# Kernel optimization log

Hardware: AMD Instinct MI355X
Metric: run time of the kernel (lower is better)

Reference implementation:

```python
import jax, jax.numpy as jnp
import numpy as np

N = 256
ACTION_DIM = 32
BATCH = 64
SEQ = 128
J0 = -0.1
J1 = 0.1
ALPHA = 0.15  # hard-coded in forward()


def _initial_bump(batch, num_neurons, bump_width_factor=10):
    # create_initial_bump with initial_angle = pi for every batch element
    angles = jnp.full((batch,), jnp.pi, dtype=jnp.float32)
    centers = (angles * num_neurons / (2.0 * jnp.pi))[:, None]          # [B,1]
    width = num_neurons / bump_width_factor
    idx = jnp.arange(num_neurons, dtype=jnp.float32)[None, :]          # [1,N]
    d = jnp.abs(idx - centers)
    dist = jnp.minimum(d, num_neurons - d)                             # circular distance
    bump = jnp.exp(-(dist ** 2) / (2.0 * width ** 2))
    return bump / jnp.linalg.norm(bump, axis=1, keepdims=True)          # [B,N]


def _w_delta7(num_neurons):
    idx = jnp.arange(num_neurons, dtype=jnp.float32)
    angle_diff = 2.0 * jnp.pi * (idx[:, None] - idx[None, :]) / num_neurons
    return jnp.cos(angle_diff)                                          # [N,N]


def setup_inputs() -> dict:
    key = jax.random.key(0)
    k1, k2, k3 = jax.random.split(key, 3)
    action_signal = jax.random.normal(k1, (BATCH, SEQ, ACTION_DIM), dtype=jnp.float32)
    scale = 1.0 / np.sqrt(N).astype(np.float32)
    Wo = jax.random.normal(k2, (N, N), dtype=jnp.float32) * scale
    Wa = jax.random.normal(k3, (ACTION_DIM, N, N), dtype=jnp.float32) * scale
    return {"action_signal": action_signal, "Wo": Wo, "Wa": Wa}


def reference(action_signal, Wo, Wa):
    B, T, A = action_signal.shape
    n = Wo.shape[0]
    r0 = _initial_bump(B, n)          # [B,N]
    Wd7 = _w_delta7(n)                # [N,N]

    def step(r, a_t):
        # W_eff = J0 + J1*Wo + sum_a a_t[:,a] * Wa[a]; recurrent = r @ W_eff
        # r @ (J0 * ones) == J0 * sum(r) broadcast -> avoid materializing [B,N,N]
        rec = (J0 * jnp.sum(r, axis=-1, keepdims=True)
               + J1 * (r @ Wo)
               + jnp.einsum('bn,anm,ba->bm', r, Wa, a_t))
        r_new = (1.0 - ALPHA) * r + ALPHA * jax.nn.relu(rec)
        return r_new, r_new

    _, bump = jax.lax.scan(step, r0, jnp.swapaxes(action_signal, 0, 1))  # [T,B,N]
    bump = jnp.swapaxes(bump, 0, 1)                                      # [B,T,N]
    r_delta7 = bump @ Wd7                                                # [B,T,N]
    r_history = r_delta7 / jnp.max(r_delta7, axis=2, keepdims=True)
    return r_history, bump
```

## Files before the change

### kernel.cpp

```cpp
#include <hip/hip_runtime.h>
#include <math.h>

#define NN 256
#define AD 32
#define BB 64
#define TT 128
#define KJ0 (-0.1f)
#define KJ1 (0.1f)
#define KALPHA 0.15f
#define BUMP_OFF (BB*TT*NN)

#define RSTR 284
#define LDS_WM   0
#define LDS_WW   32768
#define LDS_RL   33792
#define LDS_CF   38336
#define LDS_RED  38848
#define LDS_SUMR 39872
#define LDS_FLOATS 39888

#define BAR_STRIDE 64

__global__ void __launch_bounds__(256) ring_init(unsigned* bar) {
  bar[threadIdx.x] = 0u;
}

__device__ __forceinline__ void group_barrier(unsigned* g, unsigned phase) {
  __syncthreads();
  if (threadIdx.x == 0) {
    unsigned old = __hip_atomic_fetch_add(&g[0], 1u, __ATOMIC_ACQ_REL, __HIP_MEMORY_SCOPE_AGENT);
    if (old == 63u) {
      __hip_atomic_store(&g[0], 0u, __ATOMIC_RELAXED, __HIP_MEMORY_SCOPE_AGENT);
      __hip_atomic_store(&g[32], phase, __ATOMIC_RELEASE, __HIP_MEMORY_SCOPE_AGENT);
    } else {
      const unsigned long long t0 = __builtin_amdgcn_s_memrealtime();
      while (__hip_atomic_load(&g[32], __ATOMIC_RELAXED, __HIP_MEMORY_SCOPE_AGENT) < phase) {
        __builtin_amdgcn_s_sleep(2);
        if (__builtin_amdgcn_s_memrealtime() - t0 > 1000000ull) break;
      }
      (void)__hip_atomic_load(&g[32], __ATOMIC_ACQUIRE, __HIP_MEMORY_SCOPE_AGENT);
    }
  }
  __syncthreads();
}

__global__ void __launch_bounds__(1024) ring_main(const float* __restrict__ act,
                                                  const float* __restrict__ Wo,
                                                  const float* __restrict__ Wa,
                                                  float* __restrict__ out,
                                                  unsigned* __restrict__ bar) {
  extern __shared__ float sm[];
  const int tid = threadIdx.x;
  const int bid = blockIdx.x;
  const int bt = bid >> 6;
  const int mt = bid & 63;
  const int wv = tid >> 6;
  const int ln = tid & 63;
  const int bg = ln & 3;
  const int ks = wv*16 + (ln >> 2);
  const int a_idx = ks >> 3;
  const int sub = ks & 7;
  unsigned* barg = bar + bt*BAR_STRIDE;

  #pragma unroll
  for (int j = 0; j < 8; ++j) {
    const int flat = j*1024 + tid;
    const int i = flat >> 8, kk = flat & 255;
    const int a = kk >> 3, n = ((kk & 7) << 5) + i;
    const float4 w = *(const float4*)(Wa + (a*NN + n)*NN + (mt<<2));
    *(float4*)(&sm[LDS_WM + (flat<<2)]) = w;
  }
  if (tid < 256) {
    const float4 w = *(const float4*)(Wo + tid*NN + (mt<<2));
    float4 s; s.x = w.x*KJ1; s.y = w.y*KJ1; s.z = w.z*KJ1; s.w = w.w*KJ1;
    *(float4*)(&sm[LDS_WW + (tid<<2)]) = s;
  }

  {
    const int c = ln;
    float v0[4]; float ss = 0.f, sv = 0.f;
    const float denom = 2.0f*25.6f*25.6f;
    #pragma unroll
    for (int u = 0; u < 4; ++u) {
      const float fn = (float)(c*4 + u);
      const float d = fabsf(fn - 128.0f);
      const float dist = fminf(d, 256.0f - d);
      const float e = expf(-(dist*dist)/denom);
      v0[u] = e; ss += e*e; sv += e;
    }
    ss += __shfl_xor(ss,32); ss += __shfl_xor(ss,16); ss += __shfl_xor(ss,8);
    ss += __shfl_xor(ss,4);  ss += __shfl_xor(ss,2);  ss += __shfl_xor(ss,1);
    sv += __shfl_xor(sv,32); sv += __shfl_xor(sv,16); sv += __shfl_xor(sv,8);
    sv += __shfl_xor(sv,4);  sv += __shfl_xor(sv,2);  sv += __shfl_xor(sv,1);
    const float inv = 1.0f/sqrtf(ss);
    float4 o; o.x = v0[0]*inv; o.y = v0[1]*inv; o.z = v0[2]*inv; o.w = v0[3]*inv;
    *(float4*)(&sm[LDS_RL + wv*RSTR + (c<<2) + ((c>>3)<<2)]) = o;
    if (c == 0) sm[LDS_SUMR + wv] = sv*inv;
  }

  for (int t = 0; t < TT; ++t) {
    if (t > 0) {
      const float* src = out + BUMP_OFF + (((bt*16 + wv)*TT) + (t-1))*NN + (ln<<2);
      const float4 x = *(const float4*)src;
      *(float4*)(&sm[LDS_RL + wv*RSTR + (ln<<2) + ((ln>>3)<<2)]) = x;
      float s = x.x + x.y + x.z + x.w;
      s += __shfl_xor(s,32); s += __shfl_xor(s,16); s += __shfl_xor(s,8);
      s += __shfl_xor(s,4);  s += __shfl_xor(s,2);  s += __shfl_xor(s,1);
      if (ln == 0) sm[LDS_SUMR + wv] = s;
    }
    if (tid < 512) {
      const int b0 = tid >> 5, aa = tid & 31;
      sm[LDS_CF + aa*16 + b0] = act[(bt*16 + b0)*(TT*AD) + t*AD + aa];
    }
    __syncthreads();

    float acc[4][4];
    #pragma unroll
    for (int v = 0; v < 4; ++v) { acc[v][0]=0.f; acc[v][1]=0.f; acc[v][2]=0.f; acc[v][3]=0.f; }

    {
      const float4 w = *(const float4*)&sm[LDS_WW + (ks<<2)];
      const int np = ks + ((ks>>5)<<2);
      #pragma unroll
      for (int v = 0; v < 4; ++v) {
        const float rv = sm[LDS_RL + ((bg<<2)+v)*RSTR + np];
        acc[v][0] += rv*w.x; acc[v][1] += rv*w.y; acc[v][2] += rv*w.z; acc[v][3] += rv*w.w;
      }
    }

    float pacc[4][4];
    #pragma unroll
    for (int v = 0; v < 4; ++v) { pacc[v][0]=0.f; pacc[v][1]=0.f; pacc[v][2]=0.f; pacc[v][3]=0.f; }
    const float* wp  = &sm[LDS_WM + (ks<<2)];
    const float* rp0 = &sm[LDS_RL + (bg<<2)*RSTR + sub*36];
    const float* rp1 = rp0 + RSTR;
    const float* rp2 = rp1 + RSTR;
    const float* rp3 = rp2 + RSTR;
    #pragma unroll 2
    for (int i = 0; i < 32; i += 4) {
      const float4 w0 = *(const float4*)(wp + (i  )*1024);
      const float4 w1 = *(const float4*)(wp + (i+1)*1024);
      const float4 w2 = *(const float4*)(wp + (i+2)*1024);
      const float4 w3 = *(const float4*)(wp + (i+3)*1024);
      const float4 ra = *(const float4*)(rp0 + i);
      const float4 rb = *(const float4*)(rp1 + i);
      const float4 rc = *(const float4*)(rp2 + i);
      const float4 rd = *(const float4*)(rp3 + i);
      #pragma unroll
      for (int u = 0; u < 4; ++u) {
        const float4 w = (u==0)?w0:((u==1)?w1:((u==2)?w2:w3));
        const float r0v = (u==0)?ra.x:((u==1)?ra.y:((u==2)?ra.z:ra.w));
        const float r1v = (u==0)?rb.x:((u==1)?rb.y:((u==2)?rb.z:rb.w));
        const float r2v = (u==0)?rc.x:((u==1)?rc.y:((u==2)?rc.z:rc.w));
        const float r3v = (u==0)?rd.x:((u==1)?rd.y:((u==2)?rd.z:rd.w));
        pacc[0][0] += r0v*w.x; pacc[0][1] += r0v*w.y; pacc[0][2] += r0v*w.z; pacc[0][3] += r0v*w.w;
        pacc[1][0] += r1v*w.x; pacc[1][1] += r1v*w.y; pacc[1][2] += r1v*w.z; pacc[1][3] += r1v*w.w;
        pacc[2][0] += r2v*w.x; pacc[2][1] += r2v*w.y; pacc[2][2] += r2v*w.z; pacc[2][3] += r2v*w.w;
        pacc[3][0] += r3v*w.x; pacc[3][1] += r3v*w.y; pacc[3][2] += r3v*w.z; pacc[3][3] += r3v*w.w;
      }
    }
    #pragma unroll
    for (int v = 0; v < 4; ++v) {
      const float cva = sm[LDS_CF + a_idx*16 + (bg<<2) + v];
      acc[v][0] += cva*pacc[v][0]; acc[v][1] += cva*pacc[v][1];
      acc[v][2] += cva*pacc[v][2]; acc[v][3] += cva*pacc[v][3];
    }

    float vals[16];
    #pragma unroll
    for (int v = 0; v < 4; ++v) { vals[v*4+0]=acc[v][0]; vals[v*4+1]=acc[v][1];
                                  vals[v*4+2]=acc[v][2]; vals[v*4+3]=acc[v][3]; }
    { const bool hi = (ln & 32) != 0;
      #pragma unroll
      for (int j = 0; j < 8; ++j) { const float kp = hi?vals[j+8]:vals[j], sd = hi?vals[j]:vals[j+8];
        vals[j] = kp + __shfl_xor(sd, 32); } }
    { const bool hi = (ln & 16) != 0;
      #pragma unroll
      for (int j = 0; j < 4; ++j) { const float kp = hi?vals[j+4]:vals[j], sd = hi?vals[j]:vals[j+4];
        vals[j] = kp + __shfl_xor(sd, 16); } }
    { const bool hi = (ln & 8) != 0;
      #pragma unroll
      for (int j = 0; j < 2; ++j) { const float kp = hi?vals[j+2]:vals[j], sd = hi?vals[j]:vals[j+2];
        vals[j] = kp + __shfl_xor(sd, 8); } }
    { const bool hi = (ln & 4) != 0;
      { const float kp = hi?vals[1]:vals[0], sd = hi?vals[0]:vals[1];
        vals[0] = kp + __shfl_xor(sd, 4); } }
    sm[LDS_RED + wv*64 + ln] = vals[0];
    __syncthreads();

    if (wv == 0) {
      float tot = 0.f;
      #pragma unroll
      for (int w2 = 0; w2 < 16; ++w2) tot += sm[LDS_RED + w2*64 + ln];
      const int j = (((ln>>5)&1)<<3)|(((ln>>4)&1)<<2)|(((ln>>3)&1)<<1)|((ln>>2)&1);
      const int v = j >> 2, m = j & 3;
      const int b = (ln & 3)*4 + v;
      const int mm = (mt<<2) + m;
      const float rec  = tot + KJ0 * sm[LDS_SUMR + b];
      const float rold = sm[LDS_RL + b*RSTR + mm + ((mm>>5)<<2)];
      const float rnew = (1.0f-KALPHA)*rold + KALPHA*fmaxf(rec, 0.0f);
      out[BUMP_OFF + ((bt*16 + b)*TT + t)*NN + mm] = rnew;
    }
    if (t < TT-1) group_barrier(barg, (unsigned)(t+1));
  }
}

__global__ void __launch_bounds__(256) ring_epi(float* out) {
  const int b = blockIdx.x >> 7, t = blockIdx.x & 127;
  const int n = threadIdx.x;
  const int wv = threadIdx.x >> 6, ln = threadIdx.x & 63;
  __shared__ float l[12];
  const float v = out[BUMP_OFF + (b*TT + t)*NN + n];
  const float ang = (float)n * (6.283185307179586f/256.0f);
  const float cn = cosf(ang), sn = sinf(ang);
  float pc = v*cn, ps = v*sn;
  #pragma unroll
  for (int m = 32; m >= 1; m >>= 1) { pc += __shfl_xor(pc, m); ps += __shfl_xor(ps, m); }
  if (ln == 0) { l[wv] = pc; l[4+wv] = ps; }
  __syncthreads();
  const float C = l[0]+l[1]+l[2]+l[3];
  const float S = l[4]+l[5]+l[6]+l[7];
  const float d7 = C*cn + S*sn;
  float mx = d7;
  #pragma unroll
  for (int m = 32; m >= 1; m >>= 1) mx = fmaxf(mx, __shfl_xor(mx, m));
  if (ln == 0) l[8+wv] = mx;
  __syncthreads();
  mx = fmaxf(fmaxf(l[8], l[9]), fmaxf(l[10], l[11]));
  out[(b*TT + t)*NN + n] = d7/mx;
}

extern "C" void kernel_launch(void* const* d_in, const int* in_sizes, int n_in,
                              void* d_out, int out_size, void* d_ws, size_t ws_size,
                              hipStream_t stream) {
  const float* act = (const float*)d_in[0];
  const float* Wo  = (const float*)d_in[1];
  const float* Wa  = (const float*)d_in[2];
  float* outp = (float*)d_out;
  unsigned* bar = (unsigned*)d_ws;

  hipLaunchKernelGGL(ring_init, dim3(1), dim3(256), 0, stream, bar);

  (void)hipFuncSetAttribute(reinterpret_cast<const void*>(ring_main),
                            hipFuncAttributeMaxDynamicSharedMemorySize, LDS_FLOATS*4);

  hipLaunchKernelGGL(ring_main, dim3(256), dim3(1024), LDS_FLOATS*4, stream,
                     act, Wo, Wa, outp, bar);

  hipLaunchKernelGGL(ring_epi, dim3(BB*TT), dim3(256), 0, stream, outp);
}
```

Measured before the change: 1.699 ms.

## Replace counter barrier with per-block step flags polled by one wavefront

Replaces the centralized atomic-counter group barrier with per-block monotonically increasing step flags, padded to separate cache lines. Each block publishes its step with a release store. At the start of the next step, the 64 lanes of wave 0 each poll one peer block's flag. This removes the serialized atomic fetch-add contention and the last-arriver broadcast from the critical path of every timestep. The cost is 64 polling loads per block per step.

Measured after the change: 1.519 ms. -10.6%, faster.

```diff
diff --git a/kernel.cpp b/kernel.cpp
--- a/kernel.cpp
+++ b/kernel.cpp
@@ -19,36 +19,19 @@
 #define LDS_SUMR 39872
 #define LDS_FLOATS 39888
 
-#define BAR_STRIDE 64
-
-__global__ void __launch_bounds__(256) ring_init(unsigned* bar) {
-  bar[threadIdx.x] = 0u;
-}
-
-__device__ __forceinline__ void group_barrier(unsigned* g, unsigned phase) {
-  __syncthreads();
-  if (threadIdx.x == 0) {
-    unsigned old = __hip_atomic_fetch_add(&g[0], 1u, __ATOMIC_ACQ_REL, __HIP_MEMORY_SCOPE_AGENT);
-    if (old == 63u) {
-      __hip_atomic_store(&g[0], 0u, __ATOMIC_RELAXED, __HIP_MEMORY_SCOPE_AGENT);
-      __hip_atomic_store(&g[32], phase, __ATOMIC_RELEASE, __HIP_MEMORY_SCOPE_AGENT);
-    } else {
-      const unsigned long long t0 = __builtin_amdgcn_s_memrealtime();
-      while (__hip_atomic_load(&g[32], __ATOMIC_RELAXED, __HIP_MEMORY_SCOPE_AGENT) < phase) {
-        __builtin_amdgcn_s_sleep(2);
-        if (__builtin_amdgcn_s_memrealtime() - t0 > 1000000ull) break;
-      }
-      (void)__hip_atomic_load(&g[32], __ATOMIC_ACQUIRE, __HIP_MEMORY_SCOPE_AGENT);
-    }
-  }
-  __syncthreads();
+#define FPAD 32
+#define NFLAGS (4*64*FPAD)
+
+__global__ void __launch_bounds__(256) ring_init(unsigned* flags) {
+  #pragma unroll
+  for (int j = 0; j < 32; ++j) flags[j*256 + threadIdx.x] = 0u;
 }
 
 __global__ void __launch_bounds__(1024) ring_main(const float* __restrict__ act,
                                                   const float* __restrict__ Wo,
                                                   const float* __restrict__ Wa,
                                                   float* __restrict__ out,
-                                                  unsigned* __restrict__ bar) {
+                                                  unsigned* __restrict__ flags) {
   extern __shared__ float sm[];
   const int tid = threadIdx.x;
   const int bid = blockIdx.x;
@@ -60,7 +43,7 @@
   const int ks = wv*16 + (ln >> 2);
   const int a_idx = ks >> 3;
   const int sub = ks & 7;
-  unsigned* barg = bar + bt*BAR_STRIDE;
+  unsigned* myflag = flags + (bt*64 + mt)*FPAD;
 
   #pragma unroll
   for (int j = 0; j < 8; ++j) {
@@ -100,6 +83,19 @@
 
   for (int t = 0; t < TT; ++t) {
     if (t > 0) {
+      if (wv == 0) {
+        unsigned* f = flags + (bt*64 + ln)*FPAD;
+        const unsigned long long t0 = __builtin_amdgcn_s_memrealtime();
+        for (;;) {
+          const int v = (int)__hip_atomic_load(f, __ATOMIC_RELAXED, __HIP_MEMORY_SCOPE_AGENT);
+          if (v >= t) break;
+          __builtin_amdgcn_s_sleep(1);
+          if (__builtin_amdgcn_s_memrealtime() - t0 > 1000000ull) break;
+        }
+        (void)__hip_atomic_load(f, __ATOMIC_ACQUIRE, __HIP_MEMORY_SCOPE_AGENT);
+      }
+      __syncthreads();
+
       const float* src = out + BUMP_OFF + (((bt*16 + wv)*TT) + (t-1))*NN + (ln<<2);
       const float4 x = *(const float4*)src;
       *(float4*)(&sm[LDS_RL + wv*RSTR + (ln<<2) + ((ln>>3)<<2)]) = x;
@@ -201,7 +197,13 @@
       const float rnew = (1.0f-KALPHA)*rold + KALPHA*fmaxf(rec, 0.0f);
       out[BUMP_OFF + ((bt*16 + b)*TT + t)*NN + mm] = rnew;
     }
-    if (t < TT-1) group_barrier(barg, (unsigned)(t+1));
+    if (t < TT-1) {
+      __syncthreads();
+      if (tid == 0) {
+        __hip_atomic_store(myflag, (unsigned)(t+1),
+                           __ATOMIC_RELEASE, __HIP_MEMORY_SCOPE_AGENT);
+      }
+    }
   }
 }
 
@@ -237,15 +239,15 @@
   const float* Wo  = (const float*)d_in[1];
   const float* Wa  = (const float*)d_in[2];
   float* outp = (float*)d_out;
-  unsigned* bar = (unsigned*)d_ws;
-
-  hipLaunchKernelGGL(ring_init, dim3(1), dim3(256), 0, stream, bar);
+  unsigned* flags = (unsigned*)d_ws;
+
+  hipLaunchKernelGGL(ring_init, dim3(1), dim3(256), 0, stream, flags);
 
   (void)hipFuncSetAttribute(reinterpret_cast<const void*>(ring_main),
                             hipFuncAttributeMaxDynamicSharedMemorySize, LDS_FLOATS*4);
 
   hipLaunchKernelGGL(ring_main, dim3(256), dim3(1024), LDS_FLOATS*4, stream,
-                     act, Wo, Wa, outp, bar);
+                     act, Wo, Wa, outp, flags);
 
   hipLaunchKernelGGL(ring_epi, dim3(BB*TT), dim3(256), 0, stream, outp);
 }
```
